# Performance work log

Hardware: AMD Instinct MI355X
Metric: run time of the kernel (lower is better)

The kernel has to match this reference:

```python
import jax, jax.numpy as jnp
import numpy as np

N_NODES = 100000
N_EDGES = 1600000
IN_SIZE = 128
HIDDEN = 32
OUT_SIZE = 16


def _mean_agg(h, src, dst, n_nodes):
    # segment-sum of source features into destination nodes, then divide by in-degree
    summed = jax.ops.segment_sum(h[src], dst, num_segments=n_nodes)  # [N, D]
    deg = jax.ops.segment_sum(jnp.ones((src.shape[0],), h.dtype), dst, num_segments=n_nodes)
    return summed / jnp.maximum(deg, 1.0)[:, None]


def _sage_layer(h, src, dst, W_self, W_neigh, b):
    # DGL SAGEConv (mean): fc_self(h) + fc_neigh(mean_neigh(h)) + bias
    agg = _mean_agg(h, src, dst, h.shape[0])
    return h @ W_self + agg @ W_neigh + b


def setup_inputs() -> dict:
    key = jax.random.key(0)
    ks = jax.random.split(key, 9)
    inp = {
        "x": jax.random.normal(ks[0], (N_NODES, IN_SIZE), jnp.float32),
        "edge_src": jax.random.randint(ks[1], (N_EDGES,), 0, N_NODES, jnp.int32),
        "edge_dst": jax.random.randint(ks[2], (N_EDGES,), 0, N_NODES, jnp.int32),
        "W_self1": jax.random.normal(ks[3], (IN_SIZE, HIDDEN), jnp.float32) / np.sqrt(IN_SIZE),
        "W_neigh1": jax.random.normal(ks[4], (IN_SIZE, HIDDEN), jnp.float32) / np.sqrt(IN_SIZE),
        "b1": jnp.zeros((HIDDEN,), jnp.float32),
        "W_self2": jax.random.normal(ks[5], (HIDDEN, HIDDEN), jnp.float32) / np.sqrt(HIDDEN),
        "W_neigh2": jax.random.normal(ks[6], (HIDDEN, HIDDEN), jnp.float32) / np.sqrt(HIDDEN),
        "b2": jnp.zeros((HIDDEN,), jnp.float32),
        "W_self3": jax.random.normal(ks[7], (HIDDEN, OUT_SIZE), jnp.float32) / np.sqrt(HIDDEN),
        "W_neigh3": jax.random.normal(ks[8], (HIDDEN, OUT_SIZE), jnp.float32) / np.sqrt(HIDDEN),
        "b3": jnp.zeros((OUT_SIZE,), jnp.float32),
    }
    return inp


def reference(x, edge_src, edge_dst,
              W_self1, W_neigh1, b1,
              W_self2, W_neigh2, b2,
              W_self3, W_neigh3, b3):
    h = jax.nn.relu(_sage_layer(x, edge_src, edge_dst, W_self1, W_neigh1, b1))
    h = jax.nn.relu(_sage_layer(h, edge_src, edge_dst, W_self2, W_neigh2, b2))
    h = _sage_layer(h, edge_src, edge_dst, W_self3, W_neigh3, b3)
    return h
```

## Files before the change

kernel.cpp:

```cpp
#include <hip/hip_runtime.h>


#define BLOCK 256
#define NBLK 256
#define BSH 9
#define CAP 12288

typedef __attribute__((ext_vector_type(8))) short bf16x8;
typedef __attribute__((ext_vector_type(4))) float f32x4;

__device__ __forceinline__ unsigned pack_bf16(float a, float b) {
    unsigned ua = __float_as_uint(a); ua = (ua + 0x7fffu + ((ua >> 16) & 1u)) >> 16;
    unsigned ub = __float_as_uint(b); ub = (ub + 0x7fffu + ((ub >> 16) & 1u)) >> 16;
    return ua | (ub << 16);
}
__device__ __forceinline__ unsigned short bf16r(float f) {
    unsigned u = __float_as_uint(f);
    return (unsigned short)((u + 0x7fffu + ((u >> 16) & 1u)) >> 16);
}

__global__ void hist_kernel(const int* __restrict__ dst, int* __restrict__ hist,
                            int n_edges, int nbuk, int ch) {
    __shared__ int cnt[256];
    int tid = threadIdx.x;
    for (int i = tid; i < nbuk; i += BLOCK) cnt[i] = 0;
    __syncthreads();
    int e0 = blockIdx.x * ch;
    int e1 = e0 + ch; if (e1 > n_edges) e1 = n_edges;
    for (int e = e0 + tid; e < e1; e += BLOCK)
        atomicAdd(&cnt[dst[e] >> BSH], 1);
    __syncthreads();
    for (int i = tid; i < nbuk; i += BLOCK)
        hist[i * NBLK + blockIdx.x] = cnt[i];
}

__global__ void scanBlk_kernel(int* __restrict__ hist, int* __restrict__ buktot) {
    int b = blockIdx.x;
    int tid = threadIdx.x;
    int orig = hist[b * NBLK + tid];
    int v = orig;
    int lane = tid & 63, w = tid >> 6;
#pragma unroll
    for (int off = 1; off < 64; off <<= 1) {
        int u = __shfl_up(v, off);
        if (lane >= off) v += u;
    }
    __shared__ int wps[4];
    if (lane == 63) wps[w] = v;
    __syncthreads();
    int wadd = 0;
    for (int k = 0; k < w; ++k) wadd += wps[k];
    int excl = v - orig + wadd;
    hist[b * NBLK + tid] = excl;
    if (tid == 255) buktot[b] = excl + orig;
}

__global__ void scanBuk_kernel(const int* __restrict__ buktot, int* __restrict__ bukoff,
                               int nbuk, int* __restrict__ startp, int n_nodes, int n_edges) {
    int tid = threadIdx.x;
    int orig = (tid < nbuk) ? buktot[tid] : 0;
    int v = orig;
    int lane = tid & 63, w = tid >> 6;
#pragma unroll
    for (int off = 1; off < 64; off <<= 1) {
        int u = __shfl_up(v, off);
        if (lane >= off) v += u;
    }
    __shared__ int wps[4];
    if (lane == 63) wps[w] = v;
    __syncthreads();
    int wadd = 0;
    for (int k = 0; k < w; ++k) wadd += wps[k];
    int excl = v - orig + wadd;
    if (tid < nbuk) bukoff[tid] = excl;
    if (tid == 0) { bukoff[nbuk] = n_edges; startp[n_nodes] = n_edges; }
}

__global__ void part_kernel(const int* __restrict__ src, const int* __restrict__ dst,
                            const int* __restrict__ hist, const int* __restrict__ bukoff,
                            unsigned* __restrict__ pairs, int n_edges, int nbuk, int ch) {
    __shared__ int base[256];
    __shared__ int cnt[256];
    int tid = threadIdx.x;
    for (int i = tid; i < nbuk; i += BLOCK) {
        base[i] = hist[i * NBLK + blockIdx.x] + bukoff[i];
        cnt[i] = 0;
    }
    __syncthreads();
    int e0 = blockIdx.x * ch;
    int e1 = e0 + ch; if (e1 > n_edges) e1 = n_edges;
    for (int e = e0 + tid; e < e1; e += BLOCK) {
        int d = dst[e];
        int b = d >> BSH;
        unsigned dl = (unsigned)(d & ((1 << BSH) - 1));
        int r = atomicAdd(&cnt[b], 1);
        pairs[base[b] + r] = (unsigned)src[e] | (dl << 20);
    }
}

__global__ void build_kernel(const unsigned* __restrict__ pairs, const int* __restrict__ bukoff,
                             int* __restrict__ start, float* __restrict__ invdeg,
                             int* __restrict__ csr_src, int n_nodes) {
    __shared__ int deg[512];
    __shared__ int lst[512];
    __shared__ int cur[512];
    __shared__ int wps[4];
    __shared__ int scsr[CAP];

    int b = blockIdx.x;
    int tid = threadIdx.x;
    int e0 = bukoff[b];
    int e1 = bukoff[b + 1];
    int lo = b << BSH;
    int hi = lo + (1 << BSH); if (hi > n_nodes) hi = n_nodes;
    int nn = hi - lo;
    int ne = e1 - e0;

    for (int i = tid; i < 512; i += BLOCK) deg[i] = 0;
    __syncthreads();
    for (int i = e0 + tid; i < e1; i += BLOCK)
        atomicAdd(&deg[pairs[i] >> 20], 1);
    __syncthreads();

    int d0 = deg[2 * tid], d1 = deg[2 * tid + 1];
    int s = d0 + d1;
    int lane = tid & 63, w = tid >> 6;
    int v = s;
#pragma unroll
    for (int off = 1; off < 64; off <<= 1) {
        int u = __shfl_up(v, off);
        if (lane >= off) v += u;
    }
    if (lane == 63) wps[w] = v;
    __syncthreads();
    int wb = 0;
    for (int k = 0; k < w; ++k) wb += wps[k];
    int excl = wb + v - s;
    lst[2 * tid] = excl;
    lst[2 * tid + 1] = excl + d0;
    cur[2 * tid] = 0;
    cur[2 * tid + 1] = 0;
    __syncthreads();

    for (int i = tid; i < nn; i += BLOCK) {
        start[lo + i] = e0 + lst[i];
        int d = deg[i];
        invdeg[lo + i] = 1.0f / (float)(d < 1 ? 1 : d);
    }

    if (ne <= CAP) {
        for (int i = e0 + tid; i < e1; i += BLOCK) {
            unsigned pr = pairs[i];
            int dl = pr >> 20;
            int sl = lst[dl] + atomicAdd(&cur[dl], 1);
            scsr[sl] = (int)(pr & 0xFFFFFu);
        }
        __syncthreads();
        for (int i = tid; i < ne; i += BLOCK) csr_src[e0 + i] = scsr[i];
    } else {
        for (int i = e0 + tid; i < e1; i += BLOCK) {
            unsigned pr = pairs[i];
            int dl = pr >> 20;
            int sl = lst[dl] + atomicAdd(&cur[dl], 1);
            csr_src[e0 + sl] = (int)(pr & 0xFFFFFu);
        }
    }
}

__global__ void prep_kernel(const float* __restrict__ Ws1, const float* __restrict__ Wn1,
                            const float* __restrict__ Ws2, const float* __restrict__ Wn2,
                            const float* __restrict__ Ws3, const float* __restrict__ Wn3,
                            unsigned short* __restrict__ Wt1,
                            unsigned short* __restrict__ Wt2,
                            unsigned short* __restrict__ Wt3) {
    int stride = gridDim.x * BLOCK;
    int t0 = blockIdx.x * BLOCK + threadIdx.x;
    for (int i = t0; i < 64 * 128; i += stride) {
        int o = i / 128, k = i % 128;
        float v = (o < 32) ? Ws1[k * 32 + o] : Wn1[k * 32 + (o - 32)];
        Wt1[i] = bf16r(v);
    }
    for (int i = t0; i < 64 * 32; i += stride) {
        int o = i / 32, k = i % 32;
        float v = (o < 32) ? Ws2[k * 32 + o] : Wn2[k * 32 + (o - 32)];
        Wt2[i] = bf16r(v);
    }
    for (int i = t0; i < 32 * 32; i += stride) {
        int o = i / 32, k = i % 32;
        float v = (o < 16) ? Ws3[k * 16 + o] : Wn3[k * 16 + (o - 16)];
        Wt3[i] = bf16r(v);
    }
}

__global__ __launch_bounds__(256, 4)
void proj1_mfma(const float* __restrict__ x,
                const unsigned short* __restrict__ Wt,
                const float* __restrict__ bias,
                float* __restrict__ pre,
                unsigned short* __restrict__ p,
                int n_nodes) {
    int tid = threadIdx.x;
    int wv = tid >> 6, l = tid & 63;
    int col = l & 15, kg = l >> 4;
    int node0 = blockIdx.x * 64 + wv * 16;

    int arow = node0 + col;
    if (arow >= n_nodes) arow = n_nodes - 1;
    const float* xr = x + (size_t)arow * 128 + kg * 8;

    f32x4 acc[4];
#pragma unroll
    for (int t = 0; t < 4; ++t) acc[t] = (f32x4){0.f, 0.f, 0.f, 0.f};

#pragma unroll
    for (int ks = 0; ks < 4; ++ks) {
        float4 f0 = *reinterpret_cast<const float4*>(xr + ks * 32);
        float4 f1 = *reinterpret_cast<const float4*>(xr + ks * 32 + 4);
        union { bf16x8 v; unsigned u[4]; } A;
        A.u[0] = pack_bf16(f0.x, f0.y);
        A.u[1] = pack_bf16(f0.z, f0.w);
        A.u[2] = pack_bf16(f1.x, f1.y);
        A.u[3] = pack_bf16(f1.z, f1.w);
#pragma unroll
        for (int t = 0; t < 4; ++t) {
            bf16x8 B = *reinterpret_cast<const bf16x8*>(
                Wt + (size_t)(t * 16 + col) * 128 + ks * 32 + kg * 8);
            acc[t] = __builtin_amdgcn_mfma_f32_16x16x32_bf16(A.v, B, acc[t], 0, 0, 0);
        }
    }

    int nodeb = node0 + kg * 4;
#pragma unroll
    for (int t = 0; t < 4; ++t) {
        int out = t * 16 + col;
#pragma unroll
        for (int r = 0; r < 4; ++r) {
            int node = nodeb + r;
            if (node >= n_nodes) continue;
            if (t < 2) {
                pre[(size_t)node * 32 + out] = acc[t][r] + bias[out];
            } else {
                p[(size_t)node * 32 + (out - 32)] = bf16r(acc[t][r]);
            }
        }
    }
}

template<int DOUT>
__global__ __launch_bounds__(256, 4)
void proj23_mfma(const unsigned short* __restrict__ h,
                 const unsigned short* __restrict__ Wt,
                 const float* __restrict__ bias,
                 float* __restrict__ pre,
                 unsigned short* __restrict__ p,
                 int n_nodes) {
    constexpr int NTILE = DOUT / 8;
    int tid = threadIdx.x;
    int wv = tid >> 6, l = tid & 63;
    int col = l & 15, kg = l >> 4;
    int node0 = blockIdx.x * 64 + wv * 16;

    int arow = node0 + col;
    if (arow >= n_nodes) arow = n_nodes - 1;
    bf16x8 A = *reinterpret_cast<const bf16x8*>(h + (size_t)arow * 32 + kg * 8);

    f32x4 acc[NTILE];
#pragma unroll
    for (int t = 0; t < NTILE; ++t) acc[t] = (f32x4){0.f, 0.f, 0.f, 0.f};

#pragma unroll
    for (int t = 0; t < NTILE; ++t) {
        bf16x8 B = *reinterpret_cast<const bf16x8*>(
            Wt + (size_t)(t * 16 + col) * 32 + kg * 8);
        acc[t] = __builtin_amdgcn_mfma_f32_16x16x32_bf16(A, B, acc[t], 0, 0, 0);
    }

    int nodeb = node0 + kg * 4;
#pragma unroll
    for (int t = 0; t < NTILE; ++t) {
        int out = t * 16 + col;
#pragma unroll
        for (int r = 0; r < 4; ++r) {
            int node = nodeb + r;
            if (node >= n_nodes) continue;
            if (out < DOUT) {
                pre[(size_t)node * DOUT + out] = acc[t][r] + bias[out];
            } else {
                p[(size_t)node * DOUT + (out - DOUT)] = bf16r(acc[t][r]);
            }
        }
    }
}

template<int D, bool RELU, bool BF16OUT>
__global__ void gather_kernel(const unsigned short* __restrict__ p,
                              const int* __restrict__ csr_src,
                              const int* __restrict__ start,
                              const float* __restrict__ pre,
                              const float* __restrict__ invdeg,
                              void* __restrict__ outv,
                              int n_nodes) {
    constexpr int NPW = 64 / D;
    int wave = threadIdx.x >> 6;
    int lane = threadIdx.x & 63;
    int g = (blockIdx.x * (blockDim.x >> 6) + wave) * NPW + lane / D;
    int f = lane % D;
    if (g >= n_nodes) return;
    int s0 = start[g];
    int s1 = start[g + 1];
    float a0 = 0.f, a1 = 0.f, a2 = 0.f, a3 = 0.f;
    float a4 = 0.f, a5 = 0.f, a6 = 0.f, a7 = 0.f;
    int j = s0;
    for (; j + 8 <= s1; j += 8) {
        int c0 = csr_src[j + 0], c1 = csr_src[j + 1];
        int c2 = csr_src[j + 2], c3 = csr_src[j + 3];
        int c4 = csr_src[j + 4], c5 = csr_src[j + 5];
        int c6 = csr_src[j + 6], c7 = csr_src[j + 7];
        a0 += __uint_as_float((unsigned)p[(size_t)c0 * D + f] << 16);
        a1 += __uint_as_float((unsigned)p[(size_t)c1 * D + f] << 16);
        a2 += __uint_as_float((unsigned)p[(size_t)c2 * D + f] << 16);
        a3 += __uint_as_float((unsigned)p[(size_t)c3 * D + f] << 16);
        a4 += __uint_as_float((unsigned)p[(size_t)c4 * D + f] << 16);
        a5 += __uint_as_float((unsigned)p[(size_t)c5 * D + f] << 16);
        a6 += __uint_as_float((unsigned)p[(size_t)c6 * D + f] << 16);
        a7 += __uint_as_float((unsigned)p[(size_t)c7 * D + f] << 16);
    }
    for (; j + 2 <= s1; j += 2) {
        int c0 = csr_src[j], c1 = csr_src[j + 1];
        a0 += __uint_as_float((unsigned)p[(size_t)c0 * D + f] << 16);
        a1 += __uint_as_float((unsigned)p[(size_t)c1 * D + f] << 16);
    }
    if (j < s1)
        a2 += __uint_as_float((unsigned)p[(size_t)csr_src[j] * D + f] << 16);
    float a = ((a0 + a1) + (a2 + a3)) + ((a4 + a5) + (a6 + a7));
    size_t o = (size_t)g * D + f;
    float v = pre[o] + a * invdeg[g];
    if (RELU) v = fmaxf(v, 0.f);
    if (BF16OUT) {
        ((unsigned short*)outv)[o] = bf16r(v);
    } else {
        ((float*)outv)[o] = v;
    }
}

extern "C" void kernel_launch(void* const* d_in, const int* in_sizes, int n_in,
                              void* d_out, int out_size, void* d_ws, size_t ws_size,
                              hipStream_t stream) {
    const float* x        = (const float*)d_in[0];
    const int*   edge_src = (const int*)d_in[1];
    const int*   edge_dst = (const int*)d_in[2];
    const float* Ws1 = (const float*)d_in[3];
    const float* Wn1 = (const float*)d_in[4];
    const float* b1  = (const float*)d_in[5];
    const float* Ws2 = (const float*)d_in[6];
    const float* Wn2 = (const float*)d_in[7];
    const float* b2  = (const float*)d_in[8];
    const float* Ws3 = (const float*)d_in[9];
    const float* Wn3 = (const float*)d_in[10];
    const float* b3  = (const float*)d_in[11];
    float* out = (float*)d_out;

    const int IN = 128, HID = 32;
    const int n_nodes = in_sizes[0] / IN;
    const int n_edges = in_sizes[1];
    const int nbuk = (n_nodes + (1 << BSH) - 1) >> BSH;
    const int ch   = (n_edges + NBLK - 1) / NBLK;

    char* wsb = (char*)d_ws;
    size_t off = 0;
    auto alloc = [&](size_t bytes) { char* r = wsb + off; off = (off + bytes + 255) & ~(size_t)255; return r; };
    int*   startp = (int*)alloc(((size_t)n_nodes + 1) * sizeof(int));
    float* invdeg = (float*)alloc((size_t)n_nodes * sizeof(float));
    int*   csr    = (int*)alloc((size_t)n_edges * sizeof(int));
    int*   hist   = (int*)alloc((size_t)nbuk * NBLK * sizeof(int));
    int*   buktot = (int*)alloc(256 * sizeof(int));
    int*   bukoff = (int*)alloc(257 * sizeof(int));
    unsigned short* Wt1 = (unsigned short*)alloc(64 * 128 * 2);
    unsigned short* Wt2 = (unsigned short*)alloc(64 * 32 * 2);
    unsigned short* Wt3 = (unsigned short*)alloc(32 * 32 * 2);
    float* B0     = (float*)alloc((size_t)n_nodes * HID * sizeof(float));
    unsigned short* B1 = (unsigned short*)alloc((size_t)n_nodes * HID * 2);
    unsigned short* B3 = (unsigned short*)alloc((size_t)n_nodes * HID * 2);
    unsigned* pairs = (unsigned*)B0;

    const int gP     = (n_nodes + 63) / 64;
    const int gGat32 = (n_nodes + 7) / 8;
    const int gGat16 = (n_nodes + 15) / 16;

    prep_kernel   <<<64, BLOCK, 0, stream>>>(Ws1, Wn1, Ws2, Wn2, Ws3, Wn3, Wt1, Wt2, Wt3);
    hist_kernel   <<<NBLK, BLOCK, 0, stream>>>(edge_dst, hist, n_edges, nbuk, ch);
    scanBlk_kernel<<<nbuk, BLOCK, 0, stream>>>(hist, buktot);
    scanBuk_kernel<<<1, BLOCK, 0, stream>>>(buktot, bukoff, nbuk, startp, n_nodes, n_edges);
    part_kernel   <<<NBLK, BLOCK, 0, stream>>>(edge_src, edge_dst, hist, bukoff, pairs, n_edges, nbuk, ch);
    build_kernel  <<<nbuk, BLOCK, 0, stream>>>(pairs, bukoff, startp, invdeg, csr, n_nodes);

    proj1_mfma<<<gP, BLOCK, 0, stream>>>(x, Wt1, b1, B0, B1, n_nodes);
    gather_kernel<32, true, true><<<gGat32, BLOCK, 0, stream>>>(B1, csr, startp, B0, invdeg, B3, n_nodes);

    proj23_mfma<32><<<gP, BLOCK, 0, stream>>>(B3, Wt2, b2, B0, B1, n_nodes);
    gather_kernel<32, true, true><<<gGat32, BLOCK, 0, stream>>>(B1, csr, startp, B0, invdeg, B3, n_nodes);

    proj23_mfma<16><<<gP, BLOCK, 0, stream>>>(B3, Wt3, b3, B0, B1, n_nodes);
    gather_kernel<16, false, false><<<gGat16, BLOCK, 0, stream>>>(B1, csr, startp, B0, invdeg, out, n_nodes);
}
```

Before: 190.5 us.

## Fuse edge histogram with layer-1 projection, store self term in bf16, widen gather

Merges the destination histogram pass and the first-layer MFMA projection into one launch, with blocks split by index. This lets the projection overlap with CSR construction and drops a kernel launch. To make that possible, the pairs buffer gets its own allocation instead of aliasing the projection output. The self-projection intermediate is now stored in bf16 instead of fp32, halving its traffic at some cost in precision. The gather loop issues 16 independent neighbour loads per iteration to expose more memory-level parallelism, which raises register pressure.

```diff
diff --git a/kernel.cpp b/kernel.cpp
--- a/kernel.cpp
+++ b/kernel.cpp
@@ -18,20 +18,106 @@
     unsigned u = __float_as_uint(f);
     return (unsigned short)((u + 0x7fffu + ((u >> 16) & 1u)) >> 16);
 }
-
-__global__ void hist_kernel(const int* __restrict__ dst, int* __restrict__ hist,
-                            int n_edges, int nbuk, int ch) {
+__device__ __forceinline__ float bf2f(unsigned short u) {
+    return __uint_as_float((unsigned)u << 16);
+}
+
+__global__ void prep_kernel(const float* __restrict__ Ws1, const float* __restrict__ Wn1,
+                            const float* __restrict__ Ws2, const float* __restrict__ Wn2,
+                            const float* __restrict__ Ws3, const float* __restrict__ Wn3,
+                            unsigned short* __restrict__ Wt1,
+                            unsigned short* __restrict__ Wt2,
+                            unsigned short* __restrict__ Wt3) {
+    int stride = gridDim.x * BLOCK;
+    int t0 = blockIdx.x * BLOCK + threadIdx.x;
+    for (int i = t0; i < 64 * 128; i += stride) {
+        int o = i / 128, k = i % 128;
+        float v = (o < 32) ? Ws1[k * 32 + o] : Wn1[k * 32 + (o - 32)];
+        Wt1[i] = bf16r(v);
+    }
+    for (int i = t0; i < 64 * 32; i += stride) {
+        int o = i / 32, k = i % 32;
+        float v = (o < 32) ? Ws2[k * 32 + o] : Wn2[k * 32 + (o - 32)];
+        Wt2[i] = bf16r(v);
+    }
+    for (int i = t0; i < 32 * 32; i += stride) {
+        int o = i / 32, k = i % 32;
+        float v = (o < 16) ? Ws3[k * 16 + o] : Wn3[k * 16 + (o - 16)];
+        Wt3[i] = bf16r(v);
+    }
+}
+
+__global__ __launch_bounds__(256, 4)
+void stage1_kernel(const int* __restrict__ dst, int* __restrict__ hist,
+                   int n_edges, int nbuk, int ch,
+                   const float* __restrict__ x,
+                   const unsigned short* __restrict__ Wt,
+                   const float* __restrict__ bias,
+                   unsigned short* __restrict__ pre,
+                   unsigned short* __restrict__ p,
+                   int n_nodes, int nHist) {
     __shared__ int cnt[256];
-    int tid = threadIdx.x;
-    for (int i = tid; i < nbuk; i += BLOCK) cnt[i] = 0;
-    __syncthreads();
-    int e0 = blockIdx.x * ch;
-    int e1 = e0 + ch; if (e1 > n_edges) e1 = n_edges;
-    for (int e = e0 + tid; e < e1; e += BLOCK)
-        atomicAdd(&cnt[dst[e] >> BSH], 1);
-    __syncthreads();
-    for (int i = tid; i < nbuk; i += BLOCK)
-        hist[i * NBLK + blockIdx.x] = cnt[i];
+    int bid = blockIdx.x;
+    int tid = threadIdx.x;
+
+    if (bid < nHist) {
+        for (int i = tid; i < nbuk; i += BLOCK) cnt[i] = 0;
+        __syncthreads();
+        int e0 = bid * ch;
+        int e1 = e0 + ch; if (e1 > n_edges) e1 = n_edges;
+        for (int e = e0 + tid; e < e1; e += BLOCK)
+            atomicAdd(&cnt[dst[e] >> BSH], 1);
+        __syncthreads();
+        for (int i = tid; i < nbuk; i += BLOCK)
+            hist[i * NBLK + bid] = cnt[i];
+        return;
+    }
+
+    int pb = bid - nHist;
+    int wv = tid >> 6, l = tid & 63;
+    int col = l & 15, kg = l >> 4;
+    int node0 = pb * 64 + wv * 16;
+
+    int arow = node0 + col;
+    if (arow >= n_nodes) arow = n_nodes - 1;
+    const float* xr = x + (size_t)arow * 128 + kg * 8;
+
+    f32x4 acc[4];
+#pragma unroll
+    for (int t = 0; t < 4; ++t) acc[t] = (f32x4){0.f, 0.f, 0.f, 0.f};
+
+#pragma unroll
+    for (int ks = 0; ks < 4; ++ks) {
+        float4 f0 = *reinterpret_cast<const float4*>(xr + ks * 32);
+        float4 f1 = *reinterpret_cast<const float4*>(xr + ks * 32 + 4);
+        union { bf16x8 v; unsigned u[4]; } A;
+        A.u[0] = pack_bf16(f0.x, f0.y);
+        A.u[1] = pack_bf16(f0.z, f0.w);
+        A.u[2] = pack_bf16(f1.x, f1.y);
+        A.u[3] = pack_bf16(f1.z, f1.w);
+#pragma unroll
+        for (int t = 0; t < 4; ++t) {
+            bf16x8 B = *reinterpret_cast<const bf16x8*>(
+                Wt + (size_t)(t * 16 + col) * 128 + ks * 32 + kg * 8);
+            acc[t] = __builtin_amdgcn_mfma_f32_16x16x32_bf16(A.v, B, acc[t], 0, 0, 0);
+        }
+    }
+
+    int nodeb = node0 + kg * 4;
+#pragma unroll
+    for (int t = 0; t < 4; ++t) {
+        int out = t * 16 + col;
+#pragma unroll
+        for (int r = 0; r < 4; ++r) {
+            int node = nodeb + r;
+            if (node >= n_nodes) continue;
+            if (t < 2) {
+                pre[(size_t)node * 32 + out] = bf16r(acc[t][r] + bias[out]);
+            } else {
+                p[(size_t)node * 32 + (out - 32)] = bf16r(acc[t][r]);
+            }
+        }
+    }
 }
 
 __global__ void scanBlk_kernel(int* __restrict__ hist, int* __restrict__ buktot) {
@@ -167,91 +253,12 @@
     }
 }
 
-__global__ void prep_kernel(const float* __restrict__ Ws1, const float* __restrict__ Wn1,
-                            const float* __restrict__ Ws2, const float* __restrict__ Wn2,
-                            const float* __restrict__ Ws3, const float* __restrict__ Wn3,
-                            unsigned short* __restrict__ Wt1,
-                            unsigned short* __restrict__ Wt2,
-                            unsigned short* __restrict__ Wt3) {
-    int stride = gridDim.x * BLOCK;
-    int t0 = blockIdx.x * BLOCK + threadIdx.x;
-    for (int i = t0; i < 64 * 128; i += stride) {
-        int o = i / 128, k = i % 128;
-        float v = (o < 32) ? Ws1[k * 32 + o] : Wn1[k * 32 + (o - 32)];
-        Wt1[i] = bf16r(v);
-    }
-    for (int i = t0; i < 64 * 32; i += stride) {
-        int o = i / 32, k = i % 32;
-        float v = (o < 32) ? Ws2[k * 32 + o] : Wn2[k * 32 + (o - 32)];
-        Wt2[i] = bf16r(v);
-    }
-    for (int i = t0; i < 32 * 32; i += stride) {
-        int o = i / 32, k = i % 32;
-        float v = (o < 16) ? Ws3[k * 16 + o] : Wn3[k * 16 + (o - 16)];
-        Wt3[i] = bf16r(v);
-    }
-}
-
-__global__ __launch_bounds__(256, 4)
-void proj1_mfma(const float* __restrict__ x,
-                const unsigned short* __restrict__ Wt,
-                const float* __restrict__ bias,
-                float* __restrict__ pre,
-                unsigned short* __restrict__ p,
-                int n_nodes) {
-    int tid = threadIdx.x;
-    int wv = tid >> 6, l = tid & 63;
-    int col = l & 15, kg = l >> 4;
-    int node0 = blockIdx.x * 64 + wv * 16;
-
-    int arow = node0 + col;
-    if (arow >= n_nodes) arow = n_nodes - 1;
-    const float* xr = x + (size_t)arow * 128 + kg * 8;
-
-    f32x4 acc[4];
-#pragma unroll
-    for (int t = 0; t < 4; ++t) acc[t] = (f32x4){0.f, 0.f, 0.f, 0.f};
-
-#pragma unroll
-    for (int ks = 0; ks < 4; ++ks) {
-        float4 f0 = *reinterpret_cast<const float4*>(xr + ks * 32);
-        float4 f1 = *reinterpret_cast<const float4*>(xr + ks * 32 + 4);
-        union { bf16x8 v; unsigned u[4]; } A;
-        A.u[0] = pack_bf16(f0.x, f0.y);
-        A.u[1] = pack_bf16(f0.z, f0.w);
-        A.u[2] = pack_bf16(f1.x, f1.y);
-        A.u[3] = pack_bf16(f1.z, f1.w);
-#pragma unroll
-        for (int t = 0; t < 4; ++t) {
-            bf16x8 B = *reinterpret_cast<const bf16x8*>(
-                Wt + (size_t)(t * 16 + col) * 128 + ks * 32 + kg * 8);
-            acc[t] = __builtin_amdgcn_mfma_f32_16x16x32_bf16(A.v, B, acc[t], 0, 0, 0);
-        }
-    }
-
-    int nodeb = node0 + kg * 4;
-#pragma unroll
-    for (int t = 0; t < 4; ++t) {
-        int out = t * 16 + col;
-#pragma unroll
-        for (int r = 0; r < 4; ++r) {
-            int node = nodeb + r;
-            if (node >= n_nodes) continue;
-            if (t < 2) {
-                pre[(size_t)node * 32 + out] = acc[t][r] + bias[out];
-            } else {
-                p[(size_t)node * 32 + (out - 32)] = bf16r(acc[t][r]);
-            }
-        }
-    }
-}
-
 template<int DOUT>
 __global__ __launch_bounds__(256, 4)
 void proj23_mfma(const unsigned short* __restrict__ h,
                  const unsigned short* __restrict__ Wt,
                  const float* __restrict__ bias,
-                 float* __restrict__ pre,
+                 unsigned short* __restrict__ pre,
                  unsigned short* __restrict__ p,
                  int n_nodes) {
     constexpr int NTILE = DOUT / 8;
@@ -284,7 +291,7 @@
             int node = nodeb + r;
             if (node >= n_nodes) continue;
             if (out < DOUT) {
-                pre[(size_t)node * DOUT + out] = acc[t][r] + bias[out];
+                pre[(size_t)node * DOUT + out] = bf16r(acc[t][r] + bias[out]);
             } else {
                 p[(size_t)node * DOUT + (out - DOUT)] = bf16r(acc[t][r]);
             }
@@ -296,7 +303,7 @@
 __global__ void gather_kernel(const unsigned short* __restrict__ p,
                               const int* __restrict__ csr_src,
                               const int* __restrict__ start,
-                              const float* __restrict__ pre,
+                              const unsigned short* __restrict__ pre,
                               const float* __restrict__ invdeg,
                               void* __restrict__ outv,
                               int n_nodes) {
@@ -311,30 +318,35 @@
     float a0 = 0.f, a1 = 0.f, a2 = 0.f, a3 = 0.f;
     float a4 = 0.f, a5 = 0.f, a6 = 0.f, a7 = 0.f;
     int j = s0;
-    for (; j + 8 <= s1; j += 8) {
-        int c0 = csr_src[j + 0], c1 = csr_src[j + 1];
+    for (; j + 16 <= s1; j += 16) {
+        int c[16];
+#pragma unroll
+        for (int q = 0; q < 16; ++q) c[q] = csr_src[j + q];
+        unsigned short u[16];
+#pragma unroll
+        for (int q = 0; q < 16; ++q) u[q] = p[(size_t)c[q] * D + f];
+        a0 += bf2f(u[0]) + bf2f(u[8]);
+        a1 += bf2f(u[1]) + bf2f(u[9]);
+        a2 += bf2f(u[2]) + bf2f(u[10]);
+        a3 += bf2f(u[3]) + bf2f(u[11]);
+        a4 += bf2f(u[4]) + bf2f(u[12]);
+        a5 += bf2f(u[5]) + bf2f(u[13]);
+        a6 += bf2f(u[6]) + bf2f(u[14]);
+        a7 += bf2f(u[7]) + bf2f(u[15]);
+    }
+    for (; j + 4 <= s1; j += 4) {
+        int c0 = csr_src[j], c1 = csr_src[j + 1];
         int c2 = csr_src[j + 2], c3 = csr_src[j + 3];
-        int c4 = csr_src[j + 4], c5 = csr_src[j + 5];
-        int c6 = csr_src[j + 6], c7 = csr_src[j + 7];
-        a0 += __uint_as_float((unsigned)p[(size_t)c0 * D + f] << 16);
-        a1 += __uint_as_float((unsigned)p[(size_t)c1 * D + f] << 16);
-        a2 += __uint_as_float((unsigned)p[(size_t)c2 * D + f] << 16);
-        a3 += __uint_as_float((unsigned)p[(size_t)c3 * D + f] << 16);
-        a4 += __uint_as_float((unsigned)p[(size_t)c4 * D + f] << 16);
-        a5 += __uint_as_float((unsigned)p[(size_t)c5 * D + f] << 16);
-        a6 += __uint_as_float((unsigned)p[(size_t)c6 * D + f] << 16);
-        a7 += __uint_as_float((unsigned)p[(size_t)c7 * D + f] << 16);
-    }
-    for (; j + 2 <= s1; j += 2) {
-        int c0 = csr_src[j], c1 = csr_src[j + 1];
-        a0 += __uint_as_float((unsigned)p[(size_t)c0 * D + f] << 16);
-        a1 += __uint_as_float((unsigned)p[(size_t)c1 * D + f] << 16);
-    }
-    if (j < s1)
-        a2 += __uint_as_float((unsigned)p[(size_t)csr_src[j] * D + f] << 16);
+        a0 += bf2f(p[(size_t)c0 * D + f]);
+        a1 += bf2f(p[(size_t)c1 * D + f]);
+        a2 += bf2f(p[(size_t)c2 * D + f]);
+        a3 += bf2f(p[(size_t)c3 * D + f]);
+    }
+    for (; j < s1; ++j)
+        a4 += bf2f(p[(size_t)csr_src[j] * D + f]);
     float a = ((a0 + a1) + (a2 + a3)) + ((a4 + a5) + (a6 + a7));
     size_t o = (size_t)g * D + f;
-    float v = pre[o] + a * invdeg[g];
+    float v = bf2f(pre[o]) + a * invdeg[g];
     if (RELU) v = fmaxf(v, 0.f);
     if (BF16OUT) {
         ((unsigned short*)outv)[o] = bf16r(v);
@@ -378,23 +390,23 @@
     unsigned short* Wt1 = (unsigned short*)alloc(64 * 128 * 2);
     unsigned short* Wt2 = (unsigned short*)alloc(64 * 32 * 2);
     unsigned short* Wt3 = (unsigned short*)alloc(32 * 32 * 2);
-    float* B0     = (float*)alloc((size_t)n_nodes * HID * sizeof(float));
+    unsigned* pairs = (unsigned*)alloc((size_t)n_edges * sizeof(unsigned));
+    unsigned short* B0 = (unsigned short*)alloc((size_t)n_nodes * HID * 2);
     unsigned short* B1 = (unsigned short*)alloc((size_t)n_nodes * HID * 2);
     unsigned short* B3 = (unsigned short*)alloc((size_t)n_nodes * HID * 2);
-    unsigned* pairs = (unsigned*)B0;
 
     const int gP     = (n_nodes + 63) / 64;
     const int gGat32 = (n_nodes + 7) / 8;
     const int gGat16 = (n_nodes + 15) / 16;
 
-    prep_kernel   <<<64, BLOCK, 0, stream>>>(Ws1, Wn1, Ws2, Wn2, Ws3, Wn3, Wt1, Wt2, Wt3);
-    hist_kernel   <<<NBLK, BLOCK, 0, stream>>>(edge_dst, hist, n_edges, nbuk, ch);
+    prep_kernel  <<<64, BLOCK, 0, stream>>>(Ws1, Wn1, Ws2, Wn2, Ws3, Wn3, Wt1, Wt2, Wt3);
+    stage1_kernel<<<NBLK + gP, BLOCK, 0, stream>>>(edge_dst, hist, n_edges, nbuk, ch,
+                                                   x, Wt1, b1, B0, B1, n_nodes, NBLK);
     scanBlk_kernel<<<nbuk, BLOCK, 0, stream>>>(hist, buktot);
     scanBuk_kernel<<<1, BLOCK, 0, stream>>>(buktot, bukoff, nbuk, startp, n_nodes, n_edges);
     part_kernel   <<<NBLK, BLOCK, 0, stream>>>(edge_src, edge_dst, hist, bukoff, pairs, n_edges, nbuk, ch);
     build_kernel  <<<nbuk, BLOCK, 0, stream>>>(pairs, bukoff, startp, invdeg, csr, n_nodes);
 
-    proj1_mfma<<<gP, BLOCK, 0, stream>>>(x, Wt1, b1, B0, B1, n_nodes);
     gather_kernel<32, true, true><<<gGat32, BLOCK, 0, stream>>>(B1, csr, startp, B0, invdeg, B3, n_nodes);
 
     proj23_mfma<32><<<gP, BLOCK, 0, stream>>>(B3, Wt2, b2, B0, B1, n_nodes);
```

Result: no change. 188.0 us (-1.3%).
